# Optimization experiments

Measured on AMD Instinct MI355X. Metric: run time of the kernel, lower is better.

## Reference

```python
import jax, jax.numpy as jnp
import numpy as np

B, S, HID = 2, 2048, 2048
NH = 16
HD = HID // NH  # 128


def setup_inputs() -> dict:
    key = jax.random.key(0)
    ks = jax.random.split(key, 9)
    w = 0.02  # init scale to keep logits in a sane range
    return {
        "hidden_states": jax.random.normal(ks[0], (B, S, HID), dtype=jnp.float32),
        "Wq": jax.random.normal(ks[1], (HID, HID), dtype=jnp.float32) * w,
        "bq": jnp.zeros((HID,), dtype=jnp.float32),
        "Wk": jax.random.normal(ks[2], (HID, HD), dtype=jnp.float32) * w,
        "bk": jnp.zeros((HD,), dtype=jnp.float32),
        "Wv": jax.random.normal(ks[3], (HID, HD), dtype=jnp.float32) * w,
        "bv": jnp.zeros((HD,), dtype=jnp.float32),
        "Wo": jax.random.normal(ks[4], (HID, HID), dtype=jnp.float32) * w,
        "bo": jnp.zeros((HID,), dtype=jnp.float32),
    }


def reference(hidden_states, Wq, bq, Wk, bk, Wv, bv, Wo, bo):
    b, s, _ = hidden_states.shape
    # Projections (weights stored [in, out])
    q = hidden_states @ Wq + bq                      # [B,S,HID]
    k = hidden_states @ Wk + bk                      # [B,S,HD] single shared KV head
    v = hidden_states @ Wv + bv                      # [B,S,HD]
    q = q.reshape(b, s, NH, HD)                      # [B,S,H,D]
    # MQA: all query heads attend to the same K/V
    scores = jnp.einsum("bshd,btd->bhst", q, k) / jnp.sqrt(jnp.float32(HD))  # [B,H,S,S]
    probs = jax.nn.softmax(scores, axis=-1)
    attn = jnp.einsum("bhst,btd->bshd", probs, v)    # [B,S,H,D]
    attn = attn.reshape(b, s, HID)
    return attn @ Wo + bo
```

## Files before the change

### kernel.cpp

```cpp
#include <hip/hip_runtime.h>
#include <math.h>

#define BB  2
#define SS  2048
#define HID 2048
#define NH  16
#define HD  128
#define MT  (BB * SS)
#define NC  (HID + 2 * HD)
#define QK_SCALE 0.12751744f

typedef unsigned short ushort_t;
typedef unsigned int uint_t;
typedef __bf16 bf16x8 __attribute__((ext_vector_type(8)));
typedef short short8 __attribute__((ext_vector_type(8)));
typedef float f32x4 __attribute__((ext_vector_type(4)));

__device__ __forceinline__ ushort_t f2bf(float x) {
    union { float f; uint_t u; } a; a.f = x;
    return (ushort_t)((a.u + 0x7FFFu + ((a.u >> 16) & 1u)) >> 16);
}
__device__ __forceinline__ ushort_t f2bf_fast(float x) {
    union { float f; uint_t u; } a; a.f = x;
    return (ushort_t)((a.u + 0x8000u) >> 16);
}

__device__ __forceinline__ int sw_addr(int r, int c) {
    return ((r >> 1) << 6) + ((((((r & 1) << 2) | c)) ^ ((r >> 1) & 7)) << 3);
}

#define CFENCE() asm volatile("" ::: "memory")

__global__ __launch_bounds__(256) void conv_bf16_kernel(
    const float* __restrict__ in, ushort_t* __restrict__ outb)
{
    const size_t i = ((size_t)blockIdx.x * 256 + threadIdx.x) * 8;
    const float4 a = *(const float4*)&in[i];
    const float4 b = *(const float4*)&in[i + 4];
    short8 o;
    o[0] = (short)f2bf(a.x); o[1] = (short)f2bf(a.y);
    o[2] = (short)f2bf(a.z); o[3] = (short)f2bf(a.w);
    o[4] = (short)f2bf(b.x); o[5] = (short)f2bf(b.y);
    o[6] = (short)f2bf(b.z); o[7] = (short)f2bf(b.w);
    *(short8*)&outb[i] = o;
}

__global__ __launch_bounds__(256) void convT_kernel(
    const float* __restrict__ W, ushort_t* __restrict__ Th, int K, int N)
{
    __shared__ float Ts[64][65];
    const int t = threadIdx.x;
    const int k0 = blockIdx.x * 64, n0 = blockIdx.y * 64;
    const int rr = t >> 4, c4 = (t & 15) * 4;
#pragma unroll
    for (int i = 0; i < 4; i++) {
        const int k = rr + i * 16;
        const float4 v = *(const float4*)&W[(size_t)(k0 + k) * N + n0 + c4];
        Ts[k][c4 + 0] = v.x; Ts[k][c4 + 1] = v.y;
        Ts[k][c4 + 2] = v.z; Ts[k][c4 + 3] = v.w;
    }
    __syncthreads();
    const int n = t >> 2, kc = (t & 3) * 16;
    short8 hv[2];
#pragma unroll
    for (int jj = 0; jj < 16; jj++)
        hv[jj >> 3][jj & 7] = (short)f2bf(Ts[kc + jj][n]);
    const size_t ob = (size_t)(n0 + n) * K + k0 + kc;
    *(short8*)&Th[ob]     = hv[0];
    *(short8*)&Th[ob + 8] = hv[1];
}

__global__ __launch_bounds__(256) void convT_qkv_kernel(
    const float* __restrict__ Wq, const float* __restrict__ Wk,
    const float* __restrict__ Wv, ushort_t* __restrict__ Th)
{
    __shared__ float Ts[64][65];
    const int t = threadIdx.x;
    const int y = blockIdx.y;
    const float* W; int N, rowoff, ny;
    if (y < 32)      { W = Wq; N = HID; rowoff = 0;        ny = y; }
    else if (y < 34) { W = Wk; N = HD;  rowoff = HID;      ny = y - 32; }
    else             { W = Wv; N = HD;  rowoff = HID + HD; ny = y - 34; }
    const int k0 = blockIdx.x * 64, n0 = ny * 64;
    const int rr = t >> 4, c4 = (t & 15) * 4;
#pragma unroll
    for (int i = 0; i < 4; i++) {
        const int k = rr + i * 16;
        const float4 v = *(const float4*)&W[(size_t)(k0 + k) * N + n0 + c4];
        Ts[k][c4 + 0] = v.x; Ts[k][c4 + 1] = v.y;
        Ts[k][c4 + 2] = v.z; Ts[k][c4 + 3] = v.w;
    }
    __syncthreads();
    const int n = t >> 2, kc = (t & 3) * 16;
    short8 hv[2];
#pragma unroll
    for (int jj = 0; jj < 16; jj++)
        hv[jj >> 3][jj & 7] = (short)f2bf(Ts[kc + jj][n]);
    const size_t ob = (size_t)(rowoff + n0 + n) * HID + k0 + kc;
    *(short8*)&Th[ob]     = hv[0];
    *(short8*)&Th[ob + 8] = hv[1];
}

__global__ __launch_bounds__(256, 2) void gemm_qkv_kernel(
    const ushort_t* __restrict__ Ab, const ushort_t* __restrict__ WT,
    const float* __restrict__ bq, const float* __restrict__ bk,
    const float* __restrict__ bv,
    ushort_t* __restrict__ qb, ushort_t* __restrict__ kb,
    ushort_t* __restrict__ vtb)
{
    __shared__ short lds[16384];
    constexpr int AH = 0, BH = 8192;
    constexpr int K = HID;
    const int t  = threadIdx.x;
    const int wv = t >> 6, ln = t & 63;

    const int bid = blockIdx.x;
    const int sw = (bid & 7) * 72 + (bid >> 3);
    const int bx = sw % 18, by = sw / 18;
    const int row0 = by * 128, col0 = bx * 128;

    size_t agbase[4], bgbase[4];
    int    ldst[4];
#pragma unroll
    for (int i = 0; i < 4; i++) {
        const int I = wv * 4 + i;
        const int kc = I >> 3, Iw = I & 7;
        const int lrow = Iw * 8 + (ln >> 3);
        const int sb = (ln & 7) ^ (lrow & 7);
        const int rr = lrow * 2 + (sb >> 2);
        const int cc = sb & 3;
        agbase[i] = (size_t)(row0 + rr) * K + kc * 32 + cc * 8;
        bgbase[i] = (size_t)(col0 + rr) * K + kc * 32 + cc * 8;
        ldst[i] = kc * 4096 + Iw * 512;
    }

    const int wm0 = (wv & 1) * 64, wn0 = (wv >> 1) * 64;
    const int q = ln >> 4, lm = ln & 15;
    int aoff[4], boff[4];
#pragma unroll
    for (int i = 0; i < 4; i++) aoff[i] = sw_addr(wm0 + i * 16 + lm, q);
#pragma unroll
    for (int j = 0; j < 4; j++) boff[j] = sw_addr(wn0 + j * 16 + lm, q);

    f32x4 acc[4][4];
#pragma unroll
    for (int i = 0; i < 4; i++)
#pragma unroll
        for (int j = 0; j < 4; j++) acc[i][j] = 0.f;

    for (int k0 = 0; k0 < K; k0 += 64) {
        __syncthreads();
#pragma unroll
        for (int i = 0; i < 4; i++) {
            __builtin_amdgcn_global_load_lds(
                (const __attribute__((address_space(1))) void*)(Ab + agbase[i] + k0),
                (__attribute__((address_space(3))) void*)&lds[AH + ldst[i]], 16, 0, 0);
            __builtin_amdgcn_global_load_lds(
                (const __attribute__((address_space(1))) void*)(WT + bgbase[i] + k0),
                (__attribute__((address_space(3))) void*)&lds[BH + ldst[i]], 16, 0, 0);
        }
        __syncthreads();

#pragma unroll
        for (int kc = 0; kc < 2; kc++) {
            const int co = kc * 4096;
            bf16x8 ah[4], bh[4];
#pragma unroll
            for (int i = 0; i < 4; i++) ah[i] = *(const bf16x8*)&lds[AH + co + aoff[i]];
#pragma unroll
            for (int j = 0; j < 4; j++) bh[j] = *(const bf16x8*)&lds[BH + co + boff[j]];
#pragma unroll
            for (int i = 0; i < 4; i++)
#pragma unroll
                for (int j = 0; j < 4; j++)
                    acc[i][j] = __builtin_amdgcn_mfma_f32_16x16x32_bf16(ah[i], bh[j], acc[i][j], 0, 0, 0);
        }
    }

    const int mode = (col0 < HID) ? 0 : ((col0 == HID) ? 1 : 2);
    const float* bsel = (mode == 0) ? bq : ((mode == 1) ? bk : bv);
    const int noff = (mode == 0) ? 0 : ((mode == 1) ? HID : HID + HD);
    float bj[4];
#pragma unroll
    for (int j = 0; j < 4; j++) bj[j] = bsel[col0 - noff + wn0 + j * 16 + lm];
#pragma unroll
    for (int i = 0; i < 4; i++) {
        const int mb = row0 + wm0 + i * 16 + q * 4;
#pragma unroll
        for (int j = 0; j < 4; j++) {
            const int nn = col0 + wn0 + j * 16 + lm;
#pragma unroll
            for (int rr2 = 0; rr2 < 4; rr2++) {
                const float v = acc[i][j][rr2] + bj[j];
                if (mode == 0)      qb [(size_t)(mb + rr2) * HID + nn]           = f2bf_fast(v * QK_SCALE);
                else if (mode == 1) kb [(size_t)(mb + rr2) * HD + (nn - HID)]    = f2bf_fast(v);
                else                vtb[(size_t)(nn - HID - HD) * MT + mb + rr2] = f2bf_fast(v);
            }
        }
    }
}

__global__ __launch_bounds__(256, 2) void gemm_oproj_kernel(
    const ushort_t* __restrict__ Ab, const ushort_t* __restrict__ WT,
    const float* __restrict__ bias, float* __restrict__ C, int M, int N, int K)
{
    __shared__ short lds[16384];
    constexpr int AH = 0, BH = 8192;
    const int t  = threadIdx.x;
    const int wv = t >> 6, ln = t & 63;

    const int bid = blockIdx.x;
    const int sw = (bid & 7) * 64 + (bid >> 3);
    const int bx = sw % 16, by = sw / 16;
    const int row0 = by * 128, col0 = bx * 128;

    size_t agbase[4], bgbase[4];
    int    ldst[4];
#pragma unroll
    for (int i = 0; i < 4; i++) {
        const int I = wv * 4 + i;
        const int kc = I >> 3, Iw = I & 7;
        const int lrow = Iw * 8 + (ln >> 3);
        const int sb = (ln & 7) ^ (lrow & 7);
        const int rr = lrow * 2 + (sb >> 2);
        const int cc = sb & 3;
        agbase[i] = (size_t)(row0 + rr) * K + kc * 32 + cc * 8;
        bgbase[i] = (size_t)(col0 + rr) * K + kc * 32 + cc * 8;
        ldst[i] = kc * 4096 + Iw * 512;
    }

    const int wm0 = (wv & 1) * 64, wn0 = (wv >> 1) * 64;
    const int q = ln >> 4, lm = ln & 15;
    int aoff[4], boff[4];
#pragma unroll
    for (int i = 0; i < 4; i++) aoff[i] = sw_addr(wm0 + i * 16 + lm, q);
#pragma unroll
    for (int j = 0; j < 4; j++) boff[j] = sw_addr(wn0 + j * 16 + lm, q);

    f32x4 acc[4][4];
#pragma unroll
    for (int i = 0; i < 4; i++)
#pragma unroll
        for (int j = 0; j < 4; j++) acc[i][j] = 0.f;

    for (int k0 = 0; k0 < K; k0 += 64) {
        __syncthreads();
#pragma unroll
        for (int i = 0; i < 4; i++) {
            __builtin_amdgcn_global_load_lds(
                (const __attribute__((address_space(1))) void*)(Ab + agbase[i] + k0),
                (__attribute__((address_space(3))) void*)&lds[AH + ldst[i]], 16, 0, 0);
            __builtin_amdgcn_global_load_lds(
                (const __attribute__((address_space(1))) void*)(WT + bgbase[i] + k0),
                (__attribute__((address_space(3))) void*)&lds[BH + ldst[i]], 16, 0, 0);
        }
        __syncthreads();

#pragma unroll
        for (int kc = 0; kc < 2; kc++) {
            const int co = kc * 4096;
            bf16x8 ah[4], bh[4];
#pragma unroll
            for (int i = 0; i < 4; i++) ah[i] = *(const bf16x8*)&lds[AH + co + aoff[i]];
#pragma unroll
            for (int j = 0; j < 4; j++) bh[j] = *(const bf16x8*)&lds[BH + co + boff[j]];
#pragma unroll
            for (int i = 0; i < 4; i++)
#pragma unroll
                for (int j = 0; j < 4; j++)
                    acc[i][j] = __builtin_amdgcn_mfma_f32_16x16x32_bf16(ah[i], bh[j], acc[i][j], 0, 0, 0);
        }
    }

    float bj[4];
#pragma unroll
    for (int j = 0; j < 4; j++) bj[j] = bias[col0 + wn0 + j * 16 + lm];
#pragma unroll
    for (int i = 0; i < 4; i++) {
        const int mb = row0 + wm0 + i * 16 + q * 4;
#pragma unroll
        for (int j = 0; j < 4; j++) {
            const int nn = col0 + wn0 + j * 16 + lm;
#pragma unroll
            for (int rr2 = 0; rr2 < 4; rr2++)
                C[(size_t)(mb + rr2) * N + nn] = acc[i][j][rr2] + bj[j];
        }
    }
}

__global__ __launch_bounds__(256, 2) void attn_mfma_kernel(
    const ushort_t* __restrict__ qg, const ushort_t* __restrict__ kg,
    const ushort_t* __restrict__ vtg, ushort_t* Oh)
{
    __shared__ short Ks[8192], Vts[8192], Ps[8192];
    const int b = blockIdx.z, h = blockIdx.y, qt = blockIdx.x;
    const int t = threadIdx.x, wv = t >> 6, ln = t & 63;
    const int q = ln >> 4, lm = ln & 15;
    const int w32 = wv * 32;
    const int lm7 = ln & 7;

    const ushort_t* qgb = qg + (size_t)(b * SS + qt * 128) * HID + h * HD;
    bf16x8 aq[2][4];
#pragma unroll
    for (int st = 0; st < 2; st++)
#pragma unroll
        for (int ks = 0; ks < 4; ks++)
            aq[st][ks] = *(const bf16x8*)(qgb
                + (size_t)(w32 + st * 16 + lm) * HID + (((ks << 2) | q) * 8));

    const ushort_t* kgb = kg + (size_t)b * SS * HD;
    const ushort_t* vgb = vtg + b * SS;
    uint_t koff[4], voff[4];
#pragma unroll
    for (int i = 0; i < 4; i++) {
        const int I = wv * 4 + i;
        { const int r = 4 * I + (ln >> 4); const int c = (ln & 15) ^ (r & 15);
          koff[i] = (uint_t)(r * HD + c * 8); }
        { const int r = 8 * I + (ln >> 3); const int c = (ln & 7) ^ (r & 7);
          voff[i] = (uint_t)(r * MT + c * 8); }
    }

#pragma unroll
    for (int i = 0; i < 4; i++) {
        const int I = wv * 4 + i;
        __builtin_amdgcn_global_load_lds(
            (const __attribute__((address_space(1))) void*)(kgb + koff[i]),
            (__attribute__((address_space(3))) void*)&Ks[I * 512], 16, 0, 0);
    }
#pragma unroll
    for (int i = 0; i < 4; i++) {
        const int I = wv * 4 + i;
        __builtin_amdgcn_global_load_lds(
            (const __attribute__((address_space(1))) void*)(vgb + voff[i]),
            (__attribute__((address_space(3))) void*)&Vts[I * 512], 16, 0, 0);
    }

    float lrow[2][4] = {{0.f, 0.f, 0.f, 0.f}, {0.f, 0.f, 0.f, 0.f}};
    f32x4 O[2][8];
#pragma unroll
    for (int st = 0; st < 2; st++)
#pragma unroll
        for (int ct = 0; ct < 8; ct++) O[st][ct] = 0.f;

    for (int kt = 0; kt < SS; kt += 64) {
        const int more = (kt + 64 < SS);

        asm volatile("s_waitcnt vmcnt(4)" ::: "memory");
        CFENCE();
        __builtin_amdgcn_s_barrier();
        CFENCE();

        f32x4 s[2][4];
#pragma unroll
        for (int st = 0; st < 2; st++)
#pragma unroll
            for (int ct = 0; ct < 4; ct++) s[st][ct] = 0.f;
        __builtin_amdgcn_s_setprio(1);
#pragma unroll
        for (int ks = 0; ks < 4; ks++) {
#pragma unroll
            for (int ct = 0; ct < 4; ct++) {
                const int n = ct * 16 + lm;
                const bf16x8 bk = *(const bf16x8*)&Ks[n * 128 + (((ks << 2) | q) ^ (n & 15)) * 8];
                s[0][ct] = __builtin_amdgcn_mfma_f32_16x16x32_bf16(aq[0][ks], bk, s[0][ct], 0, 0, 0);
                s[1][ct] = __builtin_amdgcn_mfma_f32_16x16x32_bf16(aq[1][ks], bk, s[1][ct], 0, 0, 0);
            }
        }
        __builtin_amdgcn_s_setprio(0);

        CFENCE();
        __builtin_amdgcn_s_barrier();
        CFENCE();
        if (more) {
#pragma unroll
            for (int i = 0; i < 4; i++) {
                const int I = wv * 4 + i;
                __builtin_amdgcn_global_load_lds(
                    (const __attribute__((address_space(1))) void*)(kgb + koff[i] + (kt + 64) * HD),
                    (__attribute__((address_space(3))) void*)&Ks[I * 512], 16, 0, 0);
            }
        }

#pragma unroll
        for (int st = 0; st < 2; st++)
#pragma unroll
        for (int ct = 0; ct < 4; ct++) {
            const int ch = ct * 2 + (lm >> 3);
#pragma unroll
            for (int r = 0; r < 4; r++) {
                const float p = __builtin_amdgcn_exp2f(s[st][ct][r]);
                lrow[st][r] += p;
                const int pr = w32 + st * 16 + q * 4 + r;
                Ps[pr * 64 + ((ch ^ (pr & 7)) << 3) + lm7] = (short)f2bf_fast(p);
            }
        }

        if (more) asm volatile("s_waitcnt vmcnt(4)" ::: "memory");
        else      asm volatile("s_waitcnt vmcnt(0)" ::: "memory");
        CFENCE();
        __builtin_amdgcn_s_barrier();
        CFENCE();

        __builtin_amdgcn_s_setprio(1);
#pragma unroll
        for (int ks = 0; ks < 2; ks++) {
            const bf16x8 ap0 = *(const bf16x8*)&Ps[(w32 + lm) * 64 + (((ks << 2) | q) ^ lm7) * 8];
            const bf16x8 ap1 = *(const bf16x8*)&Ps[(w32 + 16 + lm) * 64 + (((ks << 2) | q) ^ lm7) * 8];
#pragma unroll
            for (int ct = 0; ct < 8; ct++) {
                const int d = ct * 16 + lm;
                const bf16x8 bv = *(const bf16x8*)&Vts[d * 64 + (((ks << 2) | q) ^ (d & 7)) * 8];
                O[0][ct] = __builtin_amdgcn_mfma_f32_16x16x32_bf16(ap0, bv, O[0][ct], 0, 0, 0);
                O[1][ct] = __builtin_amdgcn_mfma_f32_16x16x32_bf16(ap1, bv, O[1][ct], 0, 0, 0);
            }
        }
        __builtin_amdgcn_s_setprio(0);

        CFENCE();
        __builtin_amdgcn_s_barrier();
        CFENCE();
        if (more) {
#pragma unroll
            for (int i = 0; i < 4; i++) {
                const int I = wv * 4 + i;
                __builtin_amdgcn_global_load_lds(
                    (const __attribute__((address_space(1))) void*)(vgb + voff[i] + (kt + 64)),
                    (__attribute__((address_space(3))) void*)&Vts[I * 512], 16, 0, 0);
            }
        }
    }

#pragma unroll
    for (int msk = 1; msk < 16; msk <<= 1)
#pragma unroll
        for (int st = 0; st < 2; st++)
#pragma unroll
            for (int r = 0; r < 4; r++) lrow[st][r] += __shfl_xor(lrow[st][r], msk);
#pragma unroll
    for (int st = 0; st < 2; st++)
#pragma unroll
    for (int r = 0; r < 4; r++) {
        const float inv = 1.f / lrow[st][r];
        const size_t base = (size_t)(b * SS + qt * 128 + w32 + st * 16 + q * 4 + r) * HID + h * HD;
#pragma unroll
        for (int ct = 0; ct < 8; ct++)
            Oh[base + ct * 16 + lm] = f2bf_fast(O[st][ct][r] * inv);
    }
}

extern "C" void kernel_launch(void* const* d_in, const int* in_sizes, int n_in,
                              void* d_out, int out_size, void* d_ws, size_t ws_size,
                              hipStream_t stream)
{
    const float* hs = (const float*)d_in[0];
    const float* Wq = (const float*)d_in[1];
    const float* bq = (const float*)d_in[2];
    const float* Wk = (const float*)d_in[3];
    const float* bk = (const float*)d_in[4];
    const float* Wv = (const float*)d_in[5];
    const float* bv = (const float*)d_in[6];
    const float* Wo = (const float*)d_in[7];
    const float* bo = (const float*)d_in[8];
    float* out = (float*)d_out;

    char* w = (char*)d_ws;
    ushort_t* hsb  = (ushort_t*)w;  w += (size_t)MT * HID * 2;
    ushort_t* qb   = (ushort_t*)w;  w += (size_t)MT * HID * 2;
    ushort_t* kb   = (ushort_t*)w;  w += (size_t)MT * HD * 2;
    ushort_t* vtb  = (ushort_t*)w;  w += (size_t)HD * MT * 2;
    ushort_t* WcT  = (ushort_t*)w;  w += (size_t)NC * HID * 2;
    ushort_t* WoT  = WcT;

    conv_bf16_kernel<<<(MT * HID) / (256 * 8), 256, 0, stream>>>(hs, hsb);
    convT_qkv_kernel<<<dim3(HID / 64, 36), 256, 0, stream>>>(Wq, Wk, Wv, WcT);

    gemm_qkv_kernel<<<(NC / 128) * (MT / 128), 256, 0, stream>>>(
        hsb, WcT, bq, bk, bv, qb, kb, vtb);

    convT_kernel<<<dim3(HID / 64, HID / 64), 256, 0, stream>>>(Wo, WoT, HID, HID);

    attn_mfma_kernel<<<dim3(SS / 128, NH, BB), 256, 0, stream>>>(qb, kb, vtb, qb);

    gemm_oproj_kernel<<<(HID / 128) * (MT / 128), 256, 0, stream>>>(
        qb, WoT, bo, out, MT, HID, HID);
}
```

Baseline: 294.1 us.

## Enlarge QKV and O-proj GEMM tiles to 256x128 with 128x64 warp tiles

Both projection GEMMs move from 128x128 block tiles to 256x128. Each wave now computes a 128x64 sub-tile with 8x4 MFMA accumulators, and the LDS staging is reorganised so A covers two 128-row halves. The aim is more reuse of each loaded B fragment and less global and LDS traffic per FLOP. The cost is more LDS (48KB), more accumulator registers, which may limit occupancy under launch_bounds(256,2), and half as many blocks across the CUs.

New measurement: 319.1 us. 1.08x slower.

```diff
diff --git a/kernel.cpp b/kernel.cpp
--- a/kernel.cpp
+++ b/kernel.cpp
@@ -108,93 +108,120 @@
     ushort_t* __restrict__ qb, ushort_t* __restrict__ kb,
     ushort_t* __restrict__ vtb)
 {
-    __shared__ short lds[16384];
-    constexpr int AH = 0, BH = 8192;
+    __shared__ short lds[24576];
     constexpr int K = HID;
     const int t  = threadIdx.x;
     const int wv = t >> 6, ln = t & 63;
+    const int wm = wv >> 1, wn = wv & 1;
 
     const int bid = blockIdx.x;
-    const int sw = (bid & 7) * 72 + (bid >> 3);
+    const int sw = (bid & 7) * 36 + (bid >> 3);
     const int bx = sw % 18, by = sw / 18;
-    const int row0 = by * 128, col0 = bx * 128;
-
-    size_t agbase[4], bgbase[4];
-    int    ldst[4];
-#pragma unroll
-    for (int i = 0; i < 4; i++) {
-        const int I = wv * 4 + i;
-        const int kc = I >> 3, Iw = I & 7;
+    const int row0 = by * 256, col0 = bx * 128;
+
+    uint_t arow[2], brow[2], ccc[2];
+#pragma unroll
+    for (int j = 0; j < 2; j++) {
+        const int Iw = wv * 2 + j;
         const int lrow = Iw * 8 + (ln >> 3);
         const int sb = (ln & 7) ^ (lrow & 7);
-        const int rr = lrow * 2 + (sb >> 2);
-        const int cc = sb & 3;
-        agbase[i] = (size_t)(row0 + rr) * K + kc * 32 + cc * 8;
-        bgbase[i] = (size_t)(col0 + rr) * K + kc * 32 + cc * 8;
-        ldst[i] = kc * 4096 + Iw * 512;
-    }
-
-    const int wm0 = (wv & 1) * 64, wn0 = (wv >> 1) * 64;
+        arow[j] = (uint_t)(lrow * 2 + (sb >> 2));
+        ccc[j]  = (uint_t)((sb & 3) * 8);
+        brow[j] = arow[j];
+        (void)brow;
+    }
+    uint_t agoff[2][2], bgoff[2];
+#pragma unroll
+    for (int j = 0; j < 2; j++) {
+        agoff[0][j] = (uint_t)((row0 + arow[j]) * K) + ccc[j];
+        agoff[1][j] = (uint_t)((row0 + 128 + arow[j]) * K) + ccc[j];
+        bgoff[j]    = (uint_t)((col0 + arow[j]) * K) + ccc[j];
+    }
+    const int Iw0 = wv * 2;
+
+#define STAGE(kcol) do { \
+  _Pragma("unroll") \
+  for (int j = 0; j < 2; j++) { \
+    const int ds = (Iw0 + j) * 512; \
+    __builtin_amdgcn_global_load_lds( \
+        (const __attribute__((address_space(1))) void*)(Ab + agoff[0][j] + (kcol)), \
+        (__attribute__((address_space(3))) void*)&lds[0 * 4096 + ds], 16, 0, 0); \
+    __builtin_amdgcn_global_load_lds( \
+        (const __attribute__((address_space(1))) void*)(Ab + agoff[0][j] + (kcol) + 32), \
+        (__attribute__((address_space(3))) void*)&lds[1 * 4096 + ds], 16, 0, 0); \
+    __builtin_amdgcn_global_load_lds( \
+        (const __attribute__((address_space(1))) void*)(Ab + agoff[1][j] + (kcol)), \
+        (__attribute__((address_space(3))) void*)&lds[2 * 4096 + ds], 16, 0, 0); \
+    __builtin_amdgcn_global_load_lds( \
+        (const __attribute__((address_space(1))) void*)(Ab + agoff[1][j] + (kcol) + 32), \
+        (__attribute__((address_space(3))) void*)&lds[3 * 4096 + ds], 16, 0, 0); \
+    __builtin_amdgcn_global_load_lds( \
+        (const __attribute__((address_space(1))) void*)(WT + bgoff[j] + (kcol)), \
+        (__attribute__((address_space(3))) void*)&lds[16384 + ds], 16, 0, 0); \
+    __builtin_amdgcn_global_load_lds( \
+        (const __attribute__((address_space(1))) void*)(WT + bgoff[j] + (kcol) + 32), \
+        (__attribute__((address_space(3))) void*)&lds[16384 + 4096 + ds], 16, 0, 0); \
+  } } while (0)
+
     const int q = ln >> 4, lm = ln & 15;
-    int aoff[4], boff[4];
-#pragma unroll
-    for (int i = 0; i < 4; i++) aoff[i] = sw_addr(wm0 + i * 16 + lm, q);
-#pragma unroll
-    for (int j = 0; j < 4; j++) boff[j] = sw_addr(wn0 + j * 16 + lm, q);
-
-    f32x4 acc[4][4];
-#pragma unroll
-    for (int i = 0; i < 4; i++)
+    int aofl[8], bofl[4];
+#pragma unroll
+    for (int mf = 0; mf < 8; mf++) aofl[mf] = sw_addr(mf * 16 + lm, q);
+#pragma unroll
+    for (int nf = 0; nf < 4; nf++) bofl[nf] = sw_addr(nf * 16 + lm, q);
+
+    f32x4 acc[8][4];
+#pragma unroll
+    for (int i = 0; i < 8; i++)
 #pragma unroll
         for (int j = 0; j < 4; j++) acc[i][j] = 0.f;
+
+    const int wnb = 16384 + 0;
+#pragma unroll
+    for (int nf = 0; nf < 4; nf++) bofl[nf] = sw_addr(wn * 64 + nf * 16 + lm, q);
 
     for (int k0 = 0; k0 < K; k0 += 64) {
         __syncthreads();
-#pragma unroll
-        for (int i = 0; i < 4; i++) {
-            __builtin_amdgcn_global_load_lds(
-                (const __attribute__((address_space(1))) void*)(Ab + agbase[i] + k0),
-                (__attribute__((address_space(3))) void*)&lds[AH + ldst[i]], 16, 0, 0);
-            __builtin_amdgcn_global_load_lds(
-                (const __attribute__((address_space(1))) void*)(WT + bgbase[i] + k0),
-                (__attribute__((address_space(3))) void*)&lds[BH + ldst[i]], 16, 0, 0);
-        }
+        STAGE(k0);
         __syncthreads();
 
 #pragma unroll
         for (int kc = 0; kc < 2; kc++) {
-            const int co = kc * 4096;
-            bf16x8 ah[4], bh[4];
-#pragma unroll
-            for (int i = 0; i < 4; i++) ah[i] = *(const bf16x8*)&lds[AH + co + aoff[i]];
-#pragma unroll
-            for (int j = 0; j < 4; j++) bh[j] = *(const bf16x8*)&lds[BH + co + boff[j]];
-#pragma unroll
-            for (int i = 0; i < 4; i++)
-#pragma unroll
-                for (int j = 0; j < 4; j++)
-                    acc[i][j] = __builtin_amdgcn_mfma_f32_16x16x32_bf16(ah[i], bh[j], acc[i][j], 0, 0, 0);
-        }
-    }
+            const int ca = ((wm << 1) | kc) * 4096;
+            const int cb = wnb + kc * 4096;
+            bf16x8 ah[8], bh[4];
+#pragma unroll
+            for (int mf = 0; mf < 8; mf++) ah[mf] = *(const bf16x8*)&lds[ca + aofl[mf]];
+#pragma unroll
+            for (int nf = 0; nf < 4; nf++) bh[nf] = *(const bf16x8*)&lds[cb + bofl[nf]];
+#pragma unroll
+            for (int mf = 0; mf < 8; mf++)
+#pragma unroll
+                for (int nf = 0; nf < 4; nf++)
+                    acc[mf][nf] = __builtin_amdgcn_mfma_f32_16x16x32_bf16(
+                        ah[mf], bh[nf], acc[mf][nf], 0, 0, 0);
+        }
+    }
+#undef STAGE
 
     const int mode = (col0 < HID) ? 0 : ((col0 == HID) ? 1 : 2);
     const float* bsel = (mode == 0) ? bq : ((mode == 1) ? bk : bv);
     const int noff = (mode == 0) ? 0 : ((mode == 1) ? HID : HID + HD);
     float bj[4];
 #pragma unroll
-    for (int j = 0; j < 4; j++) bj[j] = bsel[col0 - noff + wn0 + j * 16 + lm];
-#pragma unroll
-    for (int i = 0; i < 4; i++) {
-        const int mb = row0 + wm0 + i * 16 + q * 4;
-#pragma unroll
-        for (int j = 0; j < 4; j++) {
-            const int nn = col0 + wn0 + j * 16 + lm;
-#pragma unroll
-            for (int rr2 = 0; rr2 < 4; rr2++) {
-                const float v = acc[i][j][rr2] + bj[j];
-                if (mode == 0)      qb [(size_t)(mb + rr2) * HID + nn]           = f2bf_fast(v * QK_SCALE);
-                else if (mode == 1) kb [(size_t)(mb + rr2) * HD + (nn - HID)]    = f2bf_fast(v);
-                else                vtb[(size_t)(nn - HID - HD) * MT + mb + rr2] = f2bf_fast(v);
+    for (int nf = 0; nf < 4; nf++) bj[nf] = bsel[col0 - noff + wn * 64 + nf * 16 + lm];
+#pragma unroll
+    for (int mf = 0; mf < 8; mf++) {
+        const int mb = row0 + wm * 128 + mf * 16 + q * 4;
+#pragma unroll
+        for (int nf = 0; nf < 4; nf++) {
+            const int nn = col0 + wn * 64 + nf * 16 + lm;
+#pragma unroll
+            for (int r = 0; r < 4; r++) {
+                const float v = acc[mf][nf][r] + bj[nf];
+                if (mode == 0)      qb [(size_t)(mb + r) * HID + nn]           = f2bf_fast(v * QK_SCALE);
+                else if (mode == 1) kb [(size_t)(mb + r) * HD + (nn - HID)]    = f2bf_fast(v);
+                else                vtb[(size_t)(nn - HID - HD) * MT + mb + r] = f2bf_fast(v);
             }
         }
     }
@@ -202,88 +229,110 @@
 
 __global__ __launch_bounds__(256, 2) void gemm_oproj_kernel(
     const ushort_t* __restrict__ Ab, const ushort_t* __restrict__ WT,
-    const float* __restrict__ bias, float* __restrict__ C, int M, int N, int K)
-{
-    __shared__ short lds[16384];
-    constexpr int AH = 0, BH = 8192;
+    const float* __restrict__ bias, float* __restrict__ C)
+{
+    __shared__ short lds[24576];
+    constexpr int K = HID;
     const int t  = threadIdx.x;
     const int wv = t >> 6, ln = t & 63;
+    const int wm = wv >> 1, wn = wv & 1;
 
     const int bid = blockIdx.x;
-    const int sw = (bid & 7) * 64 + (bid >> 3);
+    const int sw = (bid & 7) * 32 + (bid >> 3);
     const int bx = sw % 16, by = sw / 16;
-    const int row0 = by * 128, col0 = bx * 128;
-
-    size_t agbase[4], bgbase[4];
-    int    ldst[4];
-#pragma unroll
-    for (int i = 0; i < 4; i++) {
-        const int I = wv * 4 + i;
-        const int kc = I >> 3, Iw = I & 7;
+    const int row0 = by * 256, col0 = bx * 128;
+
+    uint_t arow[2], ccc[2];
+#pragma unroll
+    for (int j = 0; j < 2; j++) {
+        const int Iw = wv * 2 + j;
         const int lrow = Iw * 8 + (ln >> 3);
         const int sb = (ln & 7) ^ (lrow & 7);
-        const int rr = lrow * 2 + (sb >> 2);
-        const int cc = sb & 3;
-        agbase[i] = (size_t)(row0 + rr) * K + kc * 32 + cc * 8;
-        bgbase[i] = (size_t)(col0 + rr) * K + kc * 32 + cc * 8;
-        ldst[i] = kc * 4096 + Iw * 512;
-    }
-
-    const int wm0 = (wv & 1) * 64, wn0 = (wv >> 1) * 64;
+        arow[j] = (uint_t)(lrow * 2 + (sb >> 2));
+        ccc[j]  = (uint_t)((sb & 3) * 8);
+    }
+    uint_t agoff[2][2], bgoff[2];
+#pragma unroll
+    for (int j = 0; j < 2; j++) {
+        agoff[0][j] = (uint_t)((row0 + arow[j]) * K) + ccc[j];
+        agoff[1][j] = (uint_t)((row0 + 128 + arow[j]) * K) + ccc[j];
+        bgoff[j]    = (uint_t)((col0 + arow[j]) * K) + ccc[j];
+    }
+    const int Iw0 = wv * 2;
+
+#define STAGE(kcol) do { \
+  _Pragma("unroll") \
+  for (int j = 0; j < 2; j++) { \
+    const int ds = (Iw0 + j) * 512; \
+    __builtin_amdgcn_global_load_lds( \
+        (const __attribute__((address_space(1))) void*)(Ab + agoff[0][j] + (kcol)), \
+        (__attribute__((address_space(3))) void*)&lds[0 * 4096 + ds], 16, 0, 0); \
+    __builtin_amdgcn_global_load_lds( \
+        (const __attribute__((address_space(1))) void*)(Ab + agoff[0][j] + (kcol) + 32), \
+        (__attribute__((address_space(3))) void*)&lds[1 * 4096 + ds], 16, 0, 0); \
+    __builtin_amdgcn_global_load_lds( \
+        (const __attribute__((address_space(1))) void*)(Ab + agoff[1][j] + (kcol)), \
+        (__attribute__((address_space(3))) void*)&lds[2 * 4096 + ds], 16, 0, 0); \
+    __builtin_amdgcn_global_load_lds( \
+        (const __attribute__((address_space(1))) void*)(Ab + agoff[1][j] + (kcol) + 32), \
+        (__attribute__((address_space(3))) void*)&lds[3 * 4096 + ds], 16, 0, 0); \
+    __builtin_amdgcn_global_load_lds( \
+        (const __attribute__((address_space(1))) void*)(WT + bgoff[j] + (kcol)), \
+        (__attribute__((address_space(3))) void*)&lds[16384 + ds], 16, 0, 0); \
+    __builtin_amdgcn_global_load_lds( \
+        (const __attribute__((address_space(1))) void*)(WT + bgoff[j] + (kcol) + 32), \
+        (__attribute__((address_space(3))) void*)&lds[16384 + 4096 + ds], 16, 0, 0); \
+  } } while (0)
+
     const int q = ln >> 4, lm = ln & 15;
-    int aoff[4], boff[4];
-#pragma unroll
-    for (int i = 0; i < 4; i++) aoff[i] = sw_addr(wm0 + i * 16 + lm, q);
-#pragma unroll
-    for (int j = 0; j < 4; j++) boff[j] = sw_addr(wn0 + j * 16 + lm, q);
-
-    f32x4 acc[4][4];
-#pragma unroll
-    for (int i = 0; i < 4; i++)
+    int aofl[8], bofl[4];
+#pragma unroll
+    for (int mf = 0; mf < 8; mf++) aofl[mf] = sw_addr(mf * 16 + lm, q);
+#pragma unroll
+    for (int nf = 0; nf < 4; nf++) bofl[nf] = sw_addr(wn * 64 + nf * 16 + lm, q);
+
+    f32x4 acc[8][4];
+#pragma unroll
+    for (int i = 0; i < 8; i++)
 #pragma unroll
         for (int j = 0; j < 4; j++) acc[i][j] = 0.f;
 
     for (int k0 = 0; k0 < K; k0 += 64) {
         __syncthreads();
-#pragma unroll
-        for (int i = 0; i < 4; i++) {
-            __builtin_amdgcn_global_load_lds(
-                (const __attribute__((address_space(1))) void*)(Ab + agbase[i] + k0),
-                (__attribute__((address_space(3))) void*)&lds[AH + ldst[i]], 16, 0, 0);
-            __builtin_amdgcn_global_load_lds(
-                (const __attribute__((address_space(1))) void*)(WT + bgbase[i] + k0),
-                (__attribute__((address_space(3))) void*)&lds[BH + ldst[i]], 16, 0, 0);
-        }
+        STAGE(k0);
         __syncthreads();
 
 #pragma unroll
         for (int kc = 0; kc < 2; kc++) {
-            const int co = kc * 4096;
-            bf16x8 ah[4], bh[4];
-#pragma unroll
-            for (int i = 0; i < 4; i++) ah[i] = *(const bf16x8*)&lds[AH + co + aoff[i]];
-#pragma unroll
-            for (int j = 0; j < 4; j++) bh[j] = *(const bf16x8*)&lds[BH + co + boff[j]];
-#pragma unroll
-            for (int i = 0; i < 4; i++)
-#pragma unroll
-                for (int j = 0; j < 4; j++)
-                    acc[i][j] = __builtin_amdgcn_mfma_f32_16x16x32_bf16(ah[i], bh[j], acc[i][j], 0, 0, 0);
-        }
-    }
+            const int ca = ((wm << 1) | kc) * 4096;
+            const int cb = 16384 + kc * 4096;
+            bf16x8 ah[8], bh[4];
+#pragma unroll
+            for (int mf = 0; mf < 8; mf++) ah[mf] = *(const bf16x8*)&lds[ca + aofl[mf]];
+#pragma unroll
+            for (int nf = 0; nf < 4; nf++) bh[nf] = *(const bf16x8*)&lds[cb + bofl[nf]];
+#pragma unroll
+            for (int mf = 0; mf < 8; mf++)
+#pragma unroll
+                for (int nf = 0; nf < 4; nf++)
+                    acc[mf][nf] = __builtin_amdgcn_mfma_f32_16x16x32_bf16(
+                        ah[mf], bh[nf], acc[mf][nf], 0, 0, 0);
+        }
+    }
+#undef STAGE
 
     float bj[4];
 #pragma unroll
-    for (int j = 0; j < 4; j++) bj[j] = bias[col0 + wn0 + j * 16 + lm];
-#pragma unroll
-    for (int i = 0; i < 4; i++) {
-        const int mb = row0 + wm0 + i * 16 + q * 4;
-#pragma unroll
-        for (int j = 0; j < 4; j++) {
-            const int nn = col0 + wn0 + j * 16 + lm;
-#pragma unroll
-            for (int rr2 = 0; rr2 < 4; rr2++)
-                C[(size_t)(mb + rr2) * N + nn] = acc[i][j][rr2] + bj[j];
+    for (int nf = 0; nf < 4; nf++) bj[nf] = bias[col0 + wn * 64 + nf * 16 + lm];
+#pragma unroll
+    for (int mf = 0; mf < 8; mf++) {
+        const int mb = row0 + wm * 128 + mf * 16 + q * 4;
+#pragma unroll
+        for (int nf = 0; nf < 4; nf++) {
+            const int nn = col0 + wn * 64 + nf * 16 + lm;
+#pragma unroll
+            for (int r = 0; r < 4; r++)
+                C[(size_t)(mb + r) * HID + nn] = acc[mf][nf][r] + bj[nf];
         }
     }
 }
@@ -474,13 +523,13 @@
     conv_bf16_kernel<<<(MT * HID) / (256 * 8), 256, 0, stream>>>(hs, hsb);
     convT_qkv_kernel<<<dim3(HID / 64, 36), 256, 0, stream>>>(Wq, Wk, Wv, WcT);
 
-    gemm_qkv_kernel<<<(NC / 128) * (MT / 128), 256, 0, stream>>>(
+    gemm_qkv_kernel<<<(NC / 128) * (MT / 256), 256, 0, stream>>>(
         hsb, WcT, bq, bk, bv, qb, kb, vtb);
 
     convT_kernel<<<dim3(HID / 64, HID / 64), 256, 0, stream>>>(Wo, WoT, HID, HID);
 
     attn_mfma_kernel<<<dim3(SS / 128, NH, BB), 256, 0, stream>>>(qb, kb, vtb, qb);
 
-    gemm_oproj_kernel<<<(HID / 128) * (MT / 128), 256, 0, stream>>>(
-        qb, WoT, bo, out, MT, HID, HID);
-}
+    gemm_oproj_kernel<<<(HID / 128) * (MT / 256), 256, 0, stream>>>(
+        qb, WoT, bo, out);
+}
```
